# Performance work log

Hardware: AMD Instinct MI355X
Metric: run time of the kernel (lower is better)

The kernel has to match this reference:

```python
import jax, jax.numpy as jnp
import numpy as np

N = 100000        # num nodes
E2 = 3200000      # num directed edges (symmetric)
D = 256           # node feature dim
C = 40            # num classes
NIDS = 1000       # labelled node ids
TOL = 0.01
MAXITER = 16
AVG_DEG = E2 // N // 2 * 2  # ~32


def setup_inputs() -> dict:
    key = jax.random.key(0)
    k1, k2, k3, k4, k5, k6 = jax.random.split(key, 6)
    E = E2 // 2
    row_h = jax.random.randint(k1, (E,), 0, N, dtype=jnp.int32)
    col_h = jax.random.randint(k2, (E,), 0, N, dtype=jnp.int32)
    # symmetrize so I - (1-eps)*A is SPD-like (CG assumption)
    row = jnp.concatenate([row_h, col_h])
    col = jnp.concatenate([col_h, row_h])
    vals = jax.random.uniform(k3, (E,), dtype=jnp.float32) * (0.9 / 32.0)
    data = jnp.concatenate([vals, vals])
    node_features = jax.random.normal(k4, (N, D), dtype=jnp.float32)
    ids = jax.random.randint(k5, (NIDS,), 0, N, dtype=jnp.int32)
    # hk.Linear with TruncatedNormal(stddev=1/sqrt(D)) init
    W = (jax.random.truncated_normal(k6, -2.0, 2.0, (D, C), dtype=jnp.float32)
         * (1.0 / np.sqrt(D))).astype(jnp.float32)
    b = jnp.zeros((C,), jnp.float32)
    e0 = jnp.zeros((), jnp.float32)  # hk.get_parameter('e0', (), init=zeros)
    return dict(node_features=node_features, W=W, b=b, e0=e0,
                data=data, row=row, col=col, ids=ids)


def reference(node_features, W, b, e0, data, row, col, ids):
    epsilon = jax.nn.sigmoid(e0)
    # head_transform=None; d_feat > num_classes -> Linear first, then smooth
    x = node_features @ W + b  # [N, C]

    def spmv(v):  # adj @ v for COO adjacency, v: [N, C]
        return jax.ops.segment_sum(data[:, None] * v[col], row, num_segments=N)

    def f(v):  # (I - (1-eps) A) v
        return v - (1.0 - epsilon) * spmv(v)

    # smooth(): x.shape[1] (=C) <= ids.size -> direct CG on dense x, then gather ids
    sol, _ = jax.scipy.sparse.linalg.cg(f, x, tol=TOL, maxiter=MAXITER)
    return sol[ids]  # [NIDS, C] logits
```

## Files before the change

### kernel.cpp

```cpp
#include <hip/hip_runtime.h>
#include <hip/hip_fp16.h>
#include <math.h>

#define NNODE  100000
#define NEDGE  3200000
#define DFEAT  256
#define NCLS   40
#define NC_TOT 4000000
#define NIDS   1000
#define TOLSQ  1.0e-4f
#define MAXIT  16

#define SB 2048
#define SLOT_TOT 1000000
#define SPB 489
#define XB 1024
#define VT 256
#define GR     64
#define GKC    32
#define GEMM_B 1563

#define RB      128
#define NBUCK   782
#define BCAP    6144
#define SUBB    1024
#define NPB     800
#define EPB     4000

__device__ __forceinline__ float block_reduce_256(float v, float* red) {
  int tid = threadIdx.x;
  red[tid] = v;
  __syncthreads();
  #pragma unroll
  for (int off = 128; off > 0; off >>= 1) {
    if (tid < off) red[tid] += red[tid + off];
    __syncthreads();
  }
  float res = red[0];
  __syncthreads();
  return res;
}

__global__ void __launch_bounds__(256) k_pcount(const int* __restrict__ row,
                                                int* __restrict__ cntmat,
                                                int* __restrict__ total) {
  __shared__ int h[NBUCK];
  int tid = threadIdx.x, blk = blockIdx.x;
  for (int i = tid; i < NBUCK; i += 256) h[i] = 0;
  __syncthreads();
  int e0 = blk * EPB;
  for (int i = tid; i < EPB; i += 256) atomicAdd(&h[row[e0 + i] >> 7], 1);
  __syncthreads();
  for (int i = tid; i < NBUCK; i += 256) {
    int v = h[i];
    cntmat[blk * NBUCK + i] = v;
    if (v) atomicAdd(&total[i], v);
  }
}

__global__ void k_bscan2(const int* __restrict__ total, int* __restrict__ bptr) {
  __shared__ int s[1024];
  int tid = threadIdx.x;
  int v = (tid < NBUCK) ? total[tid] : 0;
  s[tid] = v;
  __syncthreads();
  for (int off = 1; off < 1024; off <<= 1) {
    int t = (tid >= off) ? s[tid - off] : 0;
    __syncthreads();
    s[tid] += t;
    __syncthreads();
  }
  if (tid < NBUCK) bptr[tid] = s[tid] - v;
  if (tid == 0) bptr[NBUCK] = NEDGE;
}

__global__ void __launch_bounds__(1024) k_colscan(int* __restrict__ cntmat,
                                                  const int* __restrict__ bptr) {
  __shared__ int s[1024];
  int b = blockIdx.x;
  int tid = threadIdx.x;
  int v = (tid < NPB) ? cntmat[tid * NBUCK + b] : 0;
  s[tid] = v;
  __syncthreads();
  for (int off = 1; off < 1024; off <<= 1) {
    int t = (tid >= off) ? s[tid - off] : 0;
    __syncthreads();
    s[tid] += t;
    __syncthreads();
  }
  if (tid < NPB) cntmat[tid * NBUCK + b] = bptr[b] + s[tid] - v;
}

__global__ void __launch_bounds__(256) k_ppart(const int* __restrict__ row,
    const int* __restrict__ col, const float* __restrict__ data,
    const int* __restrict__ offmat, uint2* __restrict__ bstage) {
  __shared__ int cnt[NBUCK];
  __shared__ int segs[NBUCK + 1];
  __shared__ int cur[NBUCK];
  __shared__ int goff[NBUCK];
  __shared__ int scp[256];
  __shared__ unsigned short bof[EPB];
  __shared__ uint2 pay[EPB];
  int tid = threadIdx.x, blk = blockIdx.x;
  int e0 = blk * EPB;

  for (int i = tid; i < NBUCK; i += 256) {
    cnt[i] = 0;
    goff[i] = offmat[blk * NBUCK + i];
  }
  __syncthreads();
  for (int i = tid; i < EPB; i += 256) atomicAdd(&cnt[row[e0 + i] >> 7], 1);
  __syncthreads();

  int t4 = tid * 4;
  int l0 = (t4 + 0 < NBUCK) ? cnt[t4 + 0] : 0;
  int l1 = (t4 + 1 < NBUCK) ? cnt[t4 + 1] : 0;
  int l2 = (t4 + 2 < NBUCK) ? cnt[t4 + 2] : 0;
  int l3 = (t4 + 3 < NBUCK) ? cnt[t4 + 3] : 0;
  int mysum = l0 + l1 + l2 + l3;
  scp[tid] = mysum;
  __syncthreads();
  for (int off = 1; off < 256; off <<= 1) {
    int t = (tid >= off) ? scp[tid - off] : 0;
    __syncthreads();
    scp[tid] += t;
    __syncthreads();
  }
  int base = scp[tid] - mysum;
  if (t4 + 0 <= NBUCK) segs[t4 + 0] = base;  base += l0;
  if (t4 + 1 <= NBUCK) segs[t4 + 1] = base;  base += l1;
  if (t4 + 2 <= NBUCK) segs[t4 + 2] = base;  base += l2;
  if (t4 + 3 <= NBUCK) segs[t4 + 3] = base;
  for (int i = tid; i < NBUCK; i += 256) cur[i] = 0;
  __syncthreads();

  for (int b = tid; b < NBUCK; b += 256) {
    int s1 = segs[b + 1];
    for (int i = segs[b]; i < s1; ++i) bof[i] = (unsigned short)b;
  }
  for (int i = tid; i < EPB; i += 256) {
    int rr = row[e0 + i];
    int b = rr >> 7;
    int rk = atomicAdd(&cur[b], 1);
    pay[segs[b] + rk] = make_uint2(((unsigned)(rr & (RB - 1)) << 17) | (unsigned)col[e0 + i],
                                   __float_as_uint(data[e0 + i]));
  }
  __syncthreads();
  for (int i = tid; i < EPB; i += 256) {
    int b = bof[i];
    bstage[goff[b] + (i - segs[b])] = pay[i];
  }
}

__global__ void __launch_bounds__(256) k_bbuild(const int* __restrict__ bptr,
    const uint2* __restrict__ bstage, int* __restrict__ rowptr,
    int2* __restrict__ csr) {
  __shared__ uint2 ebuf[BCAP];
  __shared__ int deg[SUBB];
  __shared__ int segs[SUBB];
  __shared__ int scp[256];
  int b = blockIdx.x;
  int s0 = bptr[b], s1 = bptr[b + 1];
  int n = s1 - s0;
  if (n > BCAP) n = BCAP;
  int tid = threadIdx.x;
  for (int i = tid; i < SUBB; i += 256) deg[i] = 0;
  __syncthreads();
  for (int i = tid; i < n; i += 256) {
    uint2 e = bstage[s0 + i];
    ebuf[i] = e;
    int key = (int)(e.x >> 17) * 8 + (int)((e.x & 0x1FFFF) >> 14);
    atomicAdd(&deg[key], 1);
  }
  __syncthreads();
  int t4 = tid * 4;
  int l0 = deg[t4 + 0], l1 = deg[t4 + 1], l2 = deg[t4 + 2], l3 = deg[t4 + 3];
  int mysum = l0 + l1 + l2 + l3;
  scp[tid] = mysum;
  __syncthreads();
  for (int off = 1; off < 256; off <<= 1) {
    int t = (tid >= off) ? scp[tid - off] : 0;
    __syncthreads();
    scp[tid] += t;
    __syncthreads();
  }
  int base = scp[tid] - mysum;
  segs[t4 + 0] = base;  base += l0;
  segs[t4 + 1] = base;  base += l1;
  segs[t4 + 2] = base;  base += l2;
  segs[t4 + 3] = base;
  __syncthreads();
  for (int i = tid; i < SUBB; i += 256) deg[i] = 0;
  if (tid < RB) {
    int grow = b * RB + tid;
    if (grow < NNODE) rowptr[grow] = s0 + segs[tid * 8];
  }
  if (b == 0 && tid == 0) rowptr[NNODE] = NEDGE;
  __syncthreads();
  for (int i = tid; i < n; i += 256) {
    uint2 e = ebuf[i];
    int col = (int)(e.x & 0x1FFFF);
    int key = (int)(e.x >> 17) * 8 + (col >> 14);
    int pos = atomicAdd(&deg[key], 1);
    csr[s0 + segs[key] + pos] = make_int2(col, (int)e.y);
  }
}

__global__ void __launch_bounds__(256) k_gemm(const float* __restrict__ feat,
    const float* __restrict__ W, const float* __restrict__ bias,
    float* __restrict__ r, float* __restrict__ p, __half* __restrict__ ph,
    float* __restrict__ part) {
  __shared__ float ftile[GR][GKC + 1];
  __shared__ float wtile[GKC * NCLS];
  __shared__ float red[256];
  int tid = threadIdx.x;
  int r0 = blockIdx.x * GR;
  int rl = tid >> 2;
  int cbase = (tid & 3) * 10;
  float acc[10];
  #pragma unroll
  for (int j = 0; j < 10; ++j) acc[j] = bias[cbase + j];

  for (int k0 = 0; k0 < DFEAT; k0 += GKC) {
    __syncthreads();
    #pragma unroll
    for (int it = 0; it < 2; ++it) {
      int i = tid + it * 256;
      int rr = i >> 3, kq = i & 7;
      int grow = r0 + rr;
      float4 v = make_float4(0.f, 0.f, 0.f, 0.f);
      if (grow < NNODE)
        v = *(const float4*)(feat + (size_t)grow * DFEAT + k0 + kq * 4);
      ftile[rr][kq * 4 + 0] = v.x;
      ftile[rr][kq * 4 + 1] = v.y;
      ftile[rr][kq * 4 + 2] = v.z;
      ftile[rr][kq * 4 + 3] = v.w;
    }
    #pragma unroll
    for (int it = 0; it < 5; ++it) {
      int i = tid + it * 256;
      wtile[i] = W[k0 * NCLS + i];
    }
    __syncthreads();
    #pragma unroll 4
    for (int kk = 0; kk < GKC; ++kk) {
      float f = ftile[rl][kk];
      const float* wr = &wtile[kk * NCLS + cbase];
      #pragma unroll
      for (int j = 0; j < 10; ++j) acc[j] = fmaf(f, wr[j], acc[j]);
    }
  }

  float local = 0.f;
  int g = r0 + rl;
  if (g < NNODE) {
    size_t b0 = (size_t)g * NCLS + cbase;
    #pragma unroll
    for (int j = 0; j < 10; ++j) {
      float a = acc[j];
      r[b0 + j] = a; p[b0 + j] = a; ph[b0 + j] = __float2half(a);
      local = fmaf(a, a, local);
    }
  }
  float tot = block_reduce_256(local, red);
  if (tid == 0) part[blockIdx.x] = tot;
}

__global__ void k_init_scal(const float* __restrict__ part, const float* __restrict__ e0,
                            float* __restrict__ scal) {
  __shared__ float red[256];
  float local = 0.f;
  for (int i = threadIdx.x; i < GEMM_B; i += 256) local += part[i];
  float bs = block_reduce_256(local, red);
  if (threadIdx.x == 0) {
    float eps = 1.f / (1.f + expf(-e0[0]));
    scal[0] = 1.f - eps;
    scal[1] = TOLSQ * bs;
    scal[2] = bs;
  }
}

__global__ void __launch_bounds__(VT) k_spmv(const float* __restrict__ scal, int k,
    const int* __restrict__ rowptr, const int2* __restrict__ csr,
    const __half* __restrict__ ph, const float* __restrict__ p,
    float* __restrict__ Ap, float* __restrict__ part) {
  float gamma = scal[2 + k], atol2 = scal[1];
  if (!(gamma > atol2)) return;
  float omega = scal[0];
  int b = blockIdx.x;
  int chunk = (b & 7) * (SB / 8) + (b >> 3);
  int sbase = chunk * SPB;
  float local = 0.f;
  #pragma unroll
  for (int it = 0; it < 2; ++it) {
    int li = threadIdx.x + it * VT;
    int s = sbase + li;
    if (li < SPB && s < SLOT_TOT) {
      int rr = s / 10;
      int cq4 = (s - rr * 10) * 4;
      int s0 = rowptr[rr], s1 = rowptr[rr + 1];
      float a0 = 0.f, a1 = 0.f, a2 = 0.f, a3 = 0.f;
      #pragma unroll 4
      for (int j = s0; j < s1; ++j) {
        int2 pr = csr[j];
        float w = __int_as_float(pr.y);
        uint2 g = *(const uint2*)(ph + (size_t)pr.x * NCLS + cq4);
        __half2 h01 = *(__half2*)&g.x;
        __half2 h23 = *(__half2*)&g.y;
        float2 f01 = __half22float2(h01);
        float2 f23 = __half22float2(h23);
        a0 = fmaf(w, f01.x, a0);
        a1 = fmaf(w, f01.y, a1);
        a2 = fmaf(w, f23.x, a2);
        a3 = fmaf(w, f23.y, a3);
      }
      size_t e = (size_t)rr * NCLS + cq4;
      float4 pe = *(const float4*)(p + e);
      float4 v;
      v.x = fmaf(-omega, a0, pe.x);
      v.y = fmaf(-omega, a1, pe.y);
      v.z = fmaf(-omega, a2, pe.z);
      v.w = fmaf(-omega, a3, pe.w);
      *(float4*)(Ap + e) = v;
      local = fmaf(pe.x, v.x, local);
      local = fmaf(pe.y, v.y, local);
      local = fmaf(pe.z, v.z, local);
      local = fmaf(pe.w, v.w, local);
    }
  }
  __shared__ float red[256];
  float tot = block_reduce_256(local, red);
  if (threadIdx.x == 0) part[blockIdx.x] = tot;
}

__global__ void __launch_bounds__(VT) k_xr(const float* __restrict__ scal, int k,
    const float* __restrict__ part_in,
    const float* __restrict__ p, const float* __restrict__ Ap,
    float* __restrict__ r, const int* __restrict__ ids,
    float* __restrict__ out, float* __restrict__ part_out) {
  float gamma = scal[2 + k], atol2 = scal[1];
  if (!(gamma > atol2)) return;
  __shared__ float red[256];
  float lp = 0.f;
  for (int i = threadIdx.x; i < SB; i += VT) lp += part_in[i];
  float pap = block_reduce_256(lp, red);
  float alpha = gamma / pap;
  int idx = blockIdx.x * VT + threadIdx.x;
  if (idx < NIDS * NCLS) {
    int i = idx / NCLS, c = idx - (idx / NCLS) * NCLS;
    out[idx] += alpha * p[(size_t)ids[i] * NCLS + c];
  }
  const float4* a4 = (const float4*)Ap;
  float4* r4 = (float4*)r;
  float local = 0.f;
  int stride = gridDim.x * blockDim.x;
  for (int e = blockIdx.x * blockDim.x + threadIdx.x; e < NC_TOT / 4; e += stride) {
    float4 ae = a4[e], re = r4[e];
    re.x = fmaf(-alpha, ae.x, re.x); re.y = fmaf(-alpha, ae.y, re.y);
    re.z = fmaf(-alpha, ae.z, re.z); re.w = fmaf(-alpha, ae.w, re.w);
    r4[e] = re;
    local = fmaf(re.x, re.x, local); local = fmaf(re.y, re.y, local);
    local = fmaf(re.z, re.z, local); local = fmaf(re.w, re.w, local);
  }
  float tot = block_reduce_256(local, red);
  if (threadIdx.x == 0) part_out[blockIdx.x] = tot;
}

__global__ void __launch_bounds__(VT) k_pupd(float* __restrict__ scal, int k,
    const float* __restrict__ part_in,
    const float* __restrict__ r, float* __restrict__ p, __half* __restrict__ ph) {
  float gamma = scal[2 + k], atol2 = scal[1];
  if (!(gamma > atol2)) {
    if (blockIdx.x == 0 && threadIdx.x == 0) scal[2 + k + 1] = gamma;
    return;
  }
  __shared__ float red[256];
  float lp = 0.f;
  for (int i = threadIdx.x; i < XB; i += VT) lp += part_in[i];
  float gnew = block_reduce_256(lp, red);
  float beta = gnew / gamma;
  const float4* r4 = (const float4*)r;
  float4* p4 = (float4*)p;
  int stride = gridDim.x * blockDim.x;
  for (int e = blockIdx.x * blockDim.x + threadIdx.x; e < NC_TOT / 4; e += stride) {
    float4 pe = p4[e], re = r4[e];
    pe.x = fmaf(beta, pe.x, re.x); pe.y = fmaf(beta, pe.y, re.y);
    pe.z = fmaf(beta, pe.z, re.z); pe.w = fmaf(beta, pe.w, re.w);
    p4[e] = pe;
    int e4 = e * 4;
    ph[e4 + 0] = __float2half(pe.x);
    ph[e4 + 1] = __float2half(pe.y);
    ph[e4 + 2] = __float2half(pe.z);
    ph[e4 + 3] = __float2half(pe.w);
  }
  if (blockIdx.x == 0 && threadIdx.x == 0) scal[2 + k + 1] = gnew;
}

extern "C" void kernel_launch(void* const* d_in, const int* in_sizes, int n_in,
                              void* d_out, int out_size, void* d_ws, size_t ws_size,
                              hipStream_t stream) {
  const float* feat = (const float*)d_in[0];
  const float* W    = (const float*)d_in[1];
  const float* bias = (const float*)d_in[2];
  const float* e0   = (const float*)d_in[3];
  const float* data = (const float*)d_in[4];
  const int*   row  = (const int*)d_in[5];
  const int*   col  = (const int*)d_in[6];
  const int*   ids  = (const int*)d_in[7];
  float* out = (float*)d_out;

  size_t off = 0;
  char* base = (char*)d_ws;
  auto take = [&](size_t nbytes) -> void* {
    void* ptr = base + off;
    off += (nbytes + 255) & ~(size_t)255;
    return ptr;
  };
  float* rv  = (float*)take((size_t)NC_TOT * 4);
  float* pv  = (float*)take((size_t)NC_TOT * 4);
  float* ap  = (float*)take((size_t)NC_TOT * 4);
  __half* ph = (__half*)take((size_t)NC_TOT * 2);
  int2*  csr = (int2*)take((size_t)NEDGE * 8);
  int* rowptr    = (int*)take((size_t)(NNODE + 1) * 4);
  int* cntmat    = (int*)take((size_t)NPB * NBUCK * 4);
  int* total     = (int*)take((size_t)(NBUCK + 2) * 4);
  int* bptr      = (int*)take((size_t)(NBUCK + 2) * 4);
  float* part_a  = (float*)take(SB * 4);
  float* part_b  = (float*)take(XB * 4);
  float* scal    = (float*)take(64 * 4);

  uint2* bstage = (uint2*)rv;

  hipMemsetAsync(total, 0, (size_t)(NBUCK + 2) * 4, stream);
  hipMemsetAsync(out, 0, (size_t)NIDS * NCLS * 4, stream);
  k_pcount<<<NPB, 256, 0, stream>>>(row, cntmat, total);
  k_bscan2<<<1, 1024, 0, stream>>>(total, bptr);
  k_colscan<<<NBUCK, 1024, 0, stream>>>(cntmat, bptr);
  k_ppart<<<NPB, 256, 0, stream>>>(row, col, data, cntmat, bstage);
  k_bbuild<<<NBUCK, 256, 0, stream>>>(bptr, bstage, rowptr, csr);

  k_gemm<<<GEMM_B, 256, 0, stream>>>(feat, W, bias, rv, pv, ph, part_a);
  k_init_scal<<<1, 256, 0, stream>>>(part_a, e0, scal);

  for (int k = 0; k < MAXIT; ++k) {
    k_spmv<<<SB, VT, 0, stream>>>(scal, k, rowptr, csr, ph, pv, ap, part_a);
    k_xr  <<<XB, VT, 0, stream>>>(scal, k, part_a, pv, ap, rv, ids, out, part_b);
    k_pupd<<<XB, VT, 0, stream>>>(scal, k, part_b, rv, pv, ph);
  }
}
```

Measured before the change: 444.3 us.

## Double-buffer feature tiles and read weights via scalar loads in GEMM

Reworks the dense feature×weight GEMM kernel. The feature tile is now stored transposed and double-buffered, and the next tile's global loads are issued before computing the current one. Each wavefront owns a fixed 10-class slice, marked wave-uniform with readfirstlane, so weights can come straight from global memory as scalar loads instead of being staged in LDS. The aim is to hide global load latency and remove the LDS weight staging and bank traffic, at the cost of more registers and possibly less-coalesced output stores (each lane now writes a different row).

```diff
diff --git a/kernel.cpp b/kernel.cpp
--- a/kernel.cpp
+++ b/kernel.cpp
@@ -210,49 +210,60 @@
     const float* __restrict__ W, const float* __restrict__ bias,
     float* __restrict__ r, float* __restrict__ p, __half* __restrict__ ph,
     float* __restrict__ part) {
-  __shared__ float ftile[GR][GKC + 1];
-  __shared__ float wtile[GKC * NCLS];
+  __shared__ float ftile[2][GKC][GR + 2];
   __shared__ float red[256];
   int tid = threadIdx.x;
   int r0 = blockIdx.x * GR;
-  int rl = tid >> 2;
-  int cbase = (tid & 3) * 10;
+  int lane = tid & 63;
+  int wid = tid >> 6;
+  int cbase = __builtin_amdgcn_readfirstlane(wid * 10);
+  int srr = tid >> 3, skq = tid & 7;
+  int srr1 = (tid + 256) >> 3, skq1 = (tid + 256) & 7;
   float acc[10];
   #pragma unroll
   for (int j = 0; j < 10; ++j) acc[j] = bias[cbase + j];
 
-  for (int k0 = 0; k0 < DFEAT; k0 += GKC) {
-    __syncthreads();
-    #pragma unroll
-    for (int it = 0; it < 2; ++it) {
-      int i = tid + it * 256;
-      int rr = i >> 3, kq = i & 7;
-      int grow = r0 + rr;
-      float4 v = make_float4(0.f, 0.f, 0.f, 0.f);
-      if (grow < NNODE)
-        v = *(const float4*)(feat + (size_t)grow * DFEAT + k0 + kq * 4);
-      ftile[rr][kq * 4 + 0] = v.x;
-      ftile[rr][kq * 4 + 1] = v.y;
-      ftile[rr][kq * 4 + 2] = v.z;
-      ftile[rr][kq * 4 + 3] = v.w;
+  float4 sA, sB;
+  int g0 = r0 + srr, g1 = r0 + srr1;
+  sA = make_float4(0.f, 0.f, 0.f, 0.f);
+  sB = make_float4(0.f, 0.f, 0.f, 0.f);
+  if (g0 < NNODE) sA = *(const float4*)(feat + (size_t)g0 * DFEAT + skq * 4);
+  if (g1 < NNODE) sB = *(const float4*)(feat + (size_t)g1 * DFEAT + skq1 * 4);
+  ftile[0][skq * 4 + 0][srr] = sA.x;  ftile[0][skq * 4 + 1][srr] = sA.y;
+  ftile[0][skq * 4 + 2][srr] = sA.z;  ftile[0][skq * 4 + 3][srr] = sA.w;
+  ftile[0][skq1 * 4 + 0][srr1] = sB.x;  ftile[0][skq1 * 4 + 1][srr1] = sB.y;
+  ftile[0][skq1 * 4 + 2][srr1] = sB.z;  ftile[0][skq1 * 4 + 3][srr1] = sB.w;
+  __syncthreads();
+
+  for (int t = 0; t < DFEAT / GKC; ++t) {
+    if (t + 1 < DFEAT / GKC) {
+      int k0n = (t + 1) * GKC;
+      sA = make_float4(0.f, 0.f, 0.f, 0.f);
+      sB = make_float4(0.f, 0.f, 0.f, 0.f);
+      if (g0 < NNODE) sA = *(const float4*)(feat + (size_t)g0 * DFEAT + k0n + skq * 4);
+      if (g1 < NNODE) sB = *(const float4*)(feat + (size_t)g1 * DFEAT + k0n + skq1 * 4);
     }
-    #pragma unroll
-    for (int it = 0; it < 5; ++it) {
-      int i = tid + it * 256;
-      wtile[i] = W[k0 * NCLS + i];
-    }
-    __syncthreads();
-    #pragma unroll 4
+    int k0 = t * GKC, buf = t & 1;
+    #pragma unroll 8
     for (int kk = 0; kk < GKC; ++kk) {
-      float f = ftile[rl][kk];
-      const float* wr = &wtile[kk * NCLS + cbase];
+      float f = ftile[buf][kk][lane];
+      const float* wr = W + (size_t)(k0 + kk) * NCLS + cbase;
       #pragma unroll
       for (int j = 0; j < 10; ++j) acc[j] = fmaf(f, wr[j], acc[j]);
     }
+    __syncthreads();
+    if (t + 1 < DFEAT / GKC) {
+      int nb = (t + 1) & 1;
+      ftile[nb][skq * 4 + 0][srr] = sA.x;  ftile[nb][skq * 4 + 1][srr] = sA.y;
+      ftile[nb][skq * 4 + 2][srr] = sA.z;  ftile[nb][skq * 4 + 3][srr] = sA.w;
+      ftile[nb][skq1 * 4 + 0][srr1] = sB.x;  ftile[nb][skq1 * 4 + 1][srr1] = sB.y;
+      ftile[nb][skq1 * 4 + 2][srr1] = sB.z;  ftile[nb][skq1 * 4 + 3][srr1] = sB.w;
+      __syncthreads();
+    }
   }
 
   float local = 0.f;
-  int g = r0 + rl;
+  int g = r0 + lane;
   if (g < NNODE) {
     size_t b0 = (size_t)g * NCLS + cbase;
     #pragma unroll
```

Measured after the change: 440.5 us. No clear change (-0.8%).
